# Kernel tuning notes

Hardware: AMD Instinct MI355X
Metric: run time of the kernel (lower is better)

The kernel has to match this reference:

```python
import jax, jax.numpy as jnp
import numpy as np
import math

FACTOR = 5


def setup_inputs() -> dict:
    key = jax.random.key(0)
    k1, k2, k3, k4 = jax.random.split(key, 4)
    B, L, H, D = 8, 1024, 8, 64
    S = FACTOR * math.ceil(math.log(L))  # U_part = 35
    return {
        "queries": jax.random.normal(k1, (B, L, H, D), jnp.float32),
        "keys": jax.random.normal(k2, (B, L, H, D), jnp.float32),
        "values": jax.random.normal(k3, (B, L, H, D), jnp.float32),
        "sample_idx": jax.random.randint(k4, (L, S), 0, L, dtype=jnp.int32),
        "attn_mask": 0,  # unused by the original forward
    }


def reference(queries, keys, values, sample_idx, attn_mask):
    B, L_Q, H, D = queries.shape
    L_K = keys.shape[1]
    # [B, L, H, D] -> [B, H, L, D]
    Q = jnp.transpose(queries, (0, 2, 1, 3))
    K = jnp.transpose(keys, (0, 2, 1, 3))
    V = jnpp_transpose(values) if False else jnp.transpose(values, (0, 2, 1, 3))

    u = min(FACTOR * math.ceil(math.log(L_Q)), L_Q)  # n_top

    # --- _prob_QK: sampled scores, sparsity measure, top-u query selection ---
    K_sample = K[:, :, sample_idx, :]  # [B, H, L_Q, S, D]
    QK_sample = jnp.einsum('bhqd,bhqsd->bhqs', Q, K_sample)  # [B, H, L_Q, S]
    M = QK_sample.max(axis=-1) - QK_sample.sum(axis=-1) / L_K  # [B, H, L_Q]
    _, M_top = jax.lax.top_k(M, u)  # [B, H, u]

    Q_reduce = jnp.take_along_axis(Q, M_top[..., None], axis=2)  # [B, H, u, D]
    scale = 1.0 / math.sqrt(D)
    scores_top = jnp.einsum('bhud,bhkd->bhuk', Q_reduce, K) * scale  # [B, H, u, L_K]

    # --- initial context (mask_flag=True): running causal mean of V ---
    denom = jnp.arange(1, L_K + 1, dtype=V.dtype)[:, None]  # [L_K, 1]
    context = jnp.cumsum(V, axis=2) / denom  # [B, H, L_K, D]

    # --- softmax over keys, sparse update of selected query rows ---
    attn = jax.nn.softmax(scores_top, axis=-1)  # [B, H, u, L_K]
    update = jnp.einsum('bhuk,bhkd->bhud', attn, V)  # [B, H, u, D]

    b_idx = jnp.arange(B)[:, None, None]
    h_idx = jnp.arange(H)[None, :, None]
    context = context.at[b_idx, h_idx, M_top].set(update)

    return jnp.transpose(context, (0, 2, 1, 3))  # [B, L_Q, H, D]
```

## Files before the change

### kernel.cpp

```cpp
#include <hip/hip_runtime.h>
#include <math.h>

#define BB 8
#define LL 1024
#define HH 8
#define DD 64
#define SS 35
#define UU 35
#define BH (BB*HH)
#define CH 32
#define CROWS (LL/CH)
#define NCHK 4
#define CHK 256
#define RPAD 48

#define MBLOCKS (BB*LL)
#define C1BLOCKS (BH*CH)

typedef __attribute__((ext_vector_type(8))) short short8;
typedef __attribute__((ext_vector_type(4))) float f32x4;

__device__ __forceinline__ size_t qkv_off(int b, int l, int h, int d) {
    return (((size_t)b*LL + l)*HH + h)*DD + d;
}

__device__ __forceinline__ unsigned short f2bf(float x) {
    unsigned int u = __float_as_uint(x);
    u = (u + 0x7fffu + ((u >> 16) & 1u)) >> 16;
    return (unsigned short)u;
}

__device__ __forceinline__ short8 ld_bf8_g(const float* __restrict__ p) {
    float4 x = *reinterpret_cast<const float4*>(p);
    float4 y = *reinterpret_cast<const float4*>(p + 4);
    short8 r;
    r[0] = (short)f2bf(x.x); r[1] = (short)f2bf(x.y);
    r[2] = (short)f2bf(x.z); r[3] = (short)f2bf(x.w);
    r[4] = (short)f2bf(y.x); r[5] = (short)f2bf(y.y);
    r[6] = (short)f2bf(y.z); r[7] = (short)f2bf(y.w);
    return r;
}

__device__ __forceinline__ float red8_shr(float p) {
    int t;
    t = __builtin_amdgcn_update_dpp(0, __float_as_int(p), 0x111, 0xF, 0xF, true);
    p += __int_as_float(t);
    t = __builtin_amdgcn_update_dpp(0, __float_as_int(p), 0x112, 0xF, 0xF, true);
    p += __int_as_float(t);
    t = __builtin_amdgcn_update_dpp(0, __float_as_int(p), 0x114, 0xF, 0xF, true);
    p += __int_as_float(t);
    return p;
}

__global__ __launch_bounds__(512, 2) void kernel_M_csum1(const float* __restrict__ Q,
                                                         const float* __restrict__ K,
                                                         const float* __restrict__ V,
                                                         const int*   __restrict__ sidx,
                                                         float* __restrict__ M,
                                                         float* __restrict__ csum) {
    int blk = blockIdx.x;
    if (blk < MBLOCKS) {
        __shared__ float s_mx[8][8];
        __shared__ float s_sm[8][8];
        int b = blk & 7;
        int q = blk >> 3;
        int tid = threadIdx.x;
        int w = tid >> 6, lane = tid & 63;
        int h = lane >> 3, j = lane & 7, dsub = j * 4;

        const float* qb = Q + ((size_t)(b * LL + q) * HH + h) * DD + dsub;
        f32x4 q0 = *reinterpret_cast<const f32x4*>(qb);
        f32x4 q1 = *reinterpret_cast<const f32x4*>(qb + 32);

        const int* sq = sidx + q * SS;
        int sl[5];
#pragma unroll
        for (int i = 0; i < 5; i++) {
            int s = w + 8 * i;
            sl[i] = sq[s < SS ? s : 0];
        }

        const float* kbase = K + (size_t)b * (LL * HH * DD) + h * DD + dsub;
        f32x4 ka[5], kc[5];
#pragma unroll
        for (int i = 0; i < 5; i++) {
            const float* kp = kbase + (size_t)sl[i] * (HH * DD);
            ka[i] = *reinterpret_cast<const f32x4*>(kp);
            kc[i] = *reinterpret_cast<const f32x4*>(kp + 32);
        }

        float mx = -INFINITY, sm = 0.f;
#pragma unroll
        for (int i = 0; i < 5; i++) {
            float d = q0.x * ka[i].x + q0.y * ka[i].y + q0.z * ka[i].z + q0.w * ka[i].w
                    + q1.x * kc[i].x + q1.y * kc[i].y + q1.z * kc[i].z + q1.w * kc[i].w;
            d = red8_shr(d);
            bool valid = (i < 4) || (w < 3);
            if (valid) { mx = fmaxf(mx, d); sm += d; }
        }
        if (j == 7) { s_mx[w][h] = mx; s_sm[w][h] = sm; }
        __syncthreads();
        if (tid < 8) {
            float m2 = -INFINITY, s2 = 0.f;
#pragma unroll
            for (int ww = 0; ww < 8; ww++) {
                m2 = fmaxf(m2, s_mx[ww][tid]);
                s2 += s_sm[ww][tid];
            }
            M[(b * HH + tid) * LL + q] = m2 - s2 * (1.0f / LL);
        }
    } else {
        int blk2 = blk - MBLOCKS;
        int bh = blk2 >> 5, c = blk2 & (CH - 1);
        int b = bh >> 3, h = bh & 7;
        int d = threadIdx.x & 63, seg = threadIdx.x >> 6;
        int l0 = c * CROWS + seg * 4;
        const float* vp = V + qkv_off(b, l0, h, d);
        float vr[4];
#pragma unroll
        for (int i = 0; i < 4; i++) vr[i] = vp[(size_t)i * (HH * DD)];
        float s = (vr[0] + vr[1]) + (vr[2] + vr[3]);
        __shared__ float red[8][64];
        red[seg][d] = s;
        __syncthreads();
        if (seg == 0) {
            float t = 0.f;
#pragma unroll
            for (int k = 0; k < 8; k++) t += red[k][d];
            csum[(size_t)blk2 * 64 + d] = t;
        }
    }
}

__global__ __launch_bounds__(64, 4) void kernel_topk_csum2(const float* __restrict__ M,
                                                           int* __restrict__ top,
                                                           const float* __restrict__ V,
                                                           const float* __restrict__ csum,
                                                           float* __restrict__ out) {
    if (blockIdx.x < BH) {
        int bh = blockIdx.x, lane = threadIdx.x;
        float v[16];
#pragma unroll
        for (int i = 0; i < 16; i++) v[i] = M[bh * LL + i * 64 + lane];

        for (int k = 0; k < UU; k++) {
            float bv = -INFINITY; int bi = 0x7fffffff;
#pragma unroll
            for (int i = 0; i < 16; i++) {
                if (v[i] > bv) { bv = v[i]; bi = i * 64 + lane; }
            }
#pragma unroll
            for (int w = 1; w < 64; w <<= 1) {
                float ov = __shfl_xor(bv, w);
                int   oi = __shfl_xor(bi, w);
                if (ov > bv || (ov == bv && oi < bi)) { bv = ov; bi = oi; }
            }
            if (lane == 0) top[bh * UU + k] = bi;
            if ((bi & 63) == lane) {
                int slot = bi >> 6;
#pragma unroll
                for (int i = 0; i < 16; i++) if (i == slot) v[i] = -INFINITY;
            }
        }
    } else {
        int blk = blockIdx.x - BH;
        int bh = blk >> 5, c = blk & (CH - 1);
        int b = bh >> 3, h = bh & 7;
        int d = threadIdx.x;
        int l0 = c * CROWS;
        const float* vp = V + qkv_off(b, l0, h, d);

        float vr[CROWS];
#pragma unroll
        for (int i = 0; i < CROWS; i++) vr[i] = vp[(size_t)i * (HH * DD)];

        float prefix = 0.f;
#pragma unroll
        for (int cc = 0; cc < CH; cc++) {
            float vv = csum[(size_t)(bh * CH + cc) * 64 + d];
            prefix += (cc < c) ? vv : 0.f;
        }
        float* op = out + qkv_off(b, l0, h, d);
        float run = prefix;
#pragma unroll
        for (int i = 0; i < CROWS; i++) {
            run += vr[i];
            op[(size_t)i * (HH * DD)] = run / (float)(l0 + i + 1);
        }
    }
}

__global__ __launch_bounds__(256) void kernel_attn_part(const float* __restrict__ Q,
                                                        const float* __restrict__ K,
                                                        const float* __restrict__ V,
                                                        const int*   __restrict__ top,
                                                        float* __restrict__ m_ws,
                                                        float* __restrict__ se_ws,
                                                        float* __restrict__ pv_ws) {
    __shared__ unsigned short vt[64 * CHK];
    __shared__ unsigned short p_lds[RPAD * CHK];
    __shared__ float red_m[4][RPAD];
    __shared__ float red_se[4][RPAD];
    __shared__ int   qpos_s[RPAD];

    const int blk = blockIdx.x;
    const int bh  = blk >> 2;
    const int ch  = blk & 3;
    const int b   = bh >> 3, h = bh & 7;
    const int l0  = ch * CHK;
    const int tid = threadIdx.x;
    const int w    = tid >> 6;
    const int lane = tid & 63;
    const int c    = lane & 15;
    const int g    = lane >> 4;
    const float scale = 0.125f;

    if (tid < RPAD) qpos_s[tid] = top[bh * UU + (tid < UU ? tid : UU - 1)];

#pragma unroll
    for (int i = 0; i < 8; i++) {
        int task = i * 256 + tid;
        int d   = task & 63;
        int lq8 = task >> 6;
        float vv[8];
#pragma unroll
        for (int j = 0; j < 8; j++)
            vv[j] = V[qkv_off(b, l0 + lq8 * 8 + j, h, d)];
        short8 pk;
#pragma unroll
        for (int j = 0; j < 8; j++) pk[j] = (short)f2bf(vv[j]);
        *reinterpret_cast<short8*>(vt + d * CHK + (((lq8 ^ (d & 31)) << 3))) = pk;
    }
    __syncthreads();

    f32x4 acc[3][4];
#pragma unroll
    for (int mt = 0; mt < 3; mt++)
#pragma unroll
        for (int nt = 0; nt < 4; nt++) acc[mt][nt] = (f32x4){0.f, 0.f, 0.f, 0.f};

#pragma unroll
    for (int ks = 0; ks < 2; ks++) {
        int k0 = ks * 32 + g * 8;
        short8 af[3];
#pragma unroll
        for (int mt = 0; mt < 3; mt++) {
            int row = mt * 16 + c;
            af[mt] = ld_bf8_g(Q + qkv_off(b, qpos_s[row], h, k0));
        }
#pragma unroll
        for (int nt = 0; nt < 4; nt++) {
            int kl = l0 + w * 64 + nt * 16 + c;
            short8 bf = ld_bf8_g(K + qkv_off(b, kl, h, k0));
#pragma unroll
            for (int mt = 0; mt < 3; mt++)
                acc[mt][nt] = __builtin_amdgcn_mfma_f32_16x16x32_bf16(af[mt], bf, acc[mt][nt], 0, 0, 0);
        }
    }

    float tmax[3][4];
#pragma unroll
    for (int mt = 0; mt < 3; mt++)
#pragma unroll
        for (int r = 0; r < 4; r++) {
            float m = fmaxf(fmaxf(acc[mt][0][r], acc[mt][1][r]),
                            fmaxf(acc[mt][2][r], acc[mt][3][r]));
            m = fmaxf(m, __shfl_xor(m, 1));
            m = fmaxf(m, __shfl_xor(m, 2));
            m = fmaxf(m, __shfl_xor(m, 4));
            m = fmaxf(m, __shfl_xor(m, 8));
            tmax[mt][r] = m;
        }
    if (c == 0) {
#pragma unroll
        for (int mt = 0; mt < 3; mt++)
#pragma unroll
            for (int r = 0; r < 4; r++)
                red_m[w][mt * 16 + g * 4 + r] = tmax[mt][r];
    }
    __syncthreads();

    float tse[3][4];
#pragma unroll
    for (int mt = 0; mt < 3; mt++)
#pragma unroll
        for (int r = 0; r < 4; r++) {
            int row = mt * 16 + g * 4 + r;
            float m = fmaxf(fmaxf(red_m[0][row], red_m[1][row]),
                            fmaxf(red_m[2][row], red_m[3][row]));
            float s = 0.f;
#pragma unroll
            for (int nt = 0; nt < 4; nt++) {
                float p = __expf(scale * (acc[mt][nt][r] - m));
                acc[mt][nt][r] = p;
                s += p;
                p_lds[row * CHK + w * 64 + nt * 16 + c] = f2bf(p);
            }
            s += __shfl_xor(s, 1);
            s += __shfl_xor(s, 2);
            s += __shfl_xor(s, 4);
            s += __shfl_xor(s, 8);
            tse[mt][r] = s;
        }
    if (c == 0) {
#pragma unroll
        for (int mt = 0; mt < 3; mt++)
#pragma unroll
            for (int r = 0; r < 4; r++)
                red_se[w][mt * 16 + g * 4 + r] = tse[mt][r];
    }
    __syncthreads();

    if (tid < RPAD) {
        float mm = fmaxf(fmaxf(red_m[0][tid], red_m[1][tid]),
                         fmaxf(red_m[2][tid], red_m[3][tid]));
        float ss = red_se[0][tid] + red_se[1][tid] + red_se[2][tid] + red_se[3][tid];
        m_ws[blk * RPAD + tid]  = mm;
        se_ws[blk * RPAD + tid] = ss;
    }

    f32x4 acc2[3];
#pragma unroll
    for (int mt = 0; mt < 3; mt++) acc2[mt] = (f32x4){0.f, 0.f, 0.f, 0.f};

#pragma unroll
    for (int ks = 0; ks < 8; ks++) {
        int slot = ks * 4 + g;
        int d    = w * 16 + c;
        short8 bf = *reinterpret_cast<const short8*>(
            vt + d * CHK + ((slot ^ (d & 31)) << 3));
#pragma unroll
        for (int mt = 0; mt < 3; mt++) {
            short8 af = *reinterpret_cast<const short8*>(
                p_lds + (mt * 16 + c) * CHK + ks * 32 + g * 8);
            acc2[mt] = __builtin_amdgcn_mfma_f32_16x16x32_bf16(af, bf, acc2[mt], 0, 0, 0);
        }
    }

#pragma unroll
    for (int mt = 0; mt < 3; mt++)
#pragma unroll
        for (int r = 0; r < 4; r++) {
            int row = mt * 16 + g * 4 + r;
            pv_ws[((size_t)blk * RPAD + row) * 64 + w * 16 + c] = acc2[mt][r];
        }
}

__global__ __launch_bounds__(256) void kernel_attn_comb(const int* __restrict__ top,
                                                        const float* __restrict__ m_ws,
                                                        const float* __restrict__ se_ws,
                                                        const float* __restrict__ pv_ws,
                                                        float* __restrict__ out) {
    int bh = blockIdx.x;
    int b = bh >> 3, h = bh & 7;
    const float scale = 0.125f;
    for (int idx = threadIdx.x; idx < UU * 64; idx += 256) {
        int r = idx >> 6, d = idx & 63;
        float mc[NCHK];
        float mm = -INFINITY;
#pragma unroll
        for (int ch = 0; ch < NCHK; ch++) {
            mc[ch] = m_ws[(bh * NCHK + ch) * RPAD + r];
            mm = fmaxf(mm, mc[ch]);
        }
        float num = 0.f, den = 0.f;
#pragma unroll
        for (int ch = 0; ch < NCHK; ch++) {
            float f = __expf(scale * (mc[ch] - mm));
            num += f * pv_ws[((size_t)(bh * NCHK + ch) * RPAD + r) * 64 + d];
            den += f * se_ws[(bh * NCHK + ch) * RPAD + r];
        }
        out[qkv_off(b, top[bh * UU + r], h, d)] = num / den;
    }
}

extern "C" void kernel_launch(void* const* d_in, const int* in_sizes, int n_in,
                              void* d_out, int out_size, void* d_ws, size_t ws_size,
                              hipStream_t stream) {
    const float* Q    = (const float*)d_in[0];
    const float* K    = (const float*)d_in[1];
    const float* V    = (const float*)d_in[2];
    const int*   sidx = (const int*)d_in[3];
    float* out = (float*)d_out;

    char* ws = (char*)d_ws;
    float* M     = (float*)(ws);
    int*   top   = (int*)  (ws + 262144);
    float* csum  = (float*)(ws + 271360);
    float* m_ws  = (float*)(ws + 795648);
    float* se_ws = (float*)(ws + 844800);
    float* pv_ws = (float*)(ws + 893952);

    kernel_M_csum1   <<<MBLOCKS + C1BLOCKS, 512, 0, stream>>>(Q, K, V, sidx, M, csum);
    kernel_topk_csum2<<<BH + C1BLOCKS, 64, 0, stream>>>(M, top, V, csum, out);
    kernel_attn_part <<<BH * NCHK, 256, 0, stream>>>(Q, K, V, top, m_ws, se_ws, pv_ws);
    kernel_attn_comb <<<BH, 256, 0, stream>>>(top, m_ws, se_ws, pv_ws, out);
}
```

Before: 80.89 us.

## Fuse top-k, split-K attention and combine into one online-softmax kernel; single-block cumsum

Cuts the launch chain from four kernels to two. The causal-mean cumsum now runs as 64 blocks that each scan a whole (b,h) column in 8 segments of 128 rows, and these blocks are co-scheduled with the M computation. The top-k selection is folded into the attention kernel, which runs one block per (b,h) and loops over the four key chunks with an online softmax, removing the partial-result workspace and the combine kernel. This saves launch gaps and workspace traffic. In exchange, attention parallelism drops from 256 blocks to 64, and the serial 35-step top-k plus per-chunk syncs sit on the critical path.

New measurement: 109.9 us. 35.9% more time.

```diff
diff --git a/kernel.cpp b/kernel.cpp
--- a/kernel.cpp
+++ b/kernel.cpp
@@ -8,14 +8,12 @@
 #define SS 35
 #define UU 35
 #define BH (BB*HH)
-#define CH 32
-#define CROWS (LL/CH)
 #define NCHK 4
 #define CHK 256
 #define RPAD 48
 
+#define CSBLOCKS BH
 #define MBLOCKS (BB*LL)
-#define C1BLOCKS (BH*CH)
 
 typedef __attribute__((ext_vector_type(8))) short short8;
 typedef __attribute__((ext_vector_type(4))) float f32x4;
@@ -52,18 +50,44 @@
     return p;
 }
 
-__global__ __launch_bounds__(512, 2) void kernel_M_csum1(const float* __restrict__ Q,
-                                                         const float* __restrict__ K,
-                                                         const float* __restrict__ V,
-                                                         const int*   __restrict__ sidx,
-                                                         float* __restrict__ M,
-                                                         float* __restrict__ csum) {
+__global__ __launch_bounds__(512, 2) void kernel_M_cumsum(const float* __restrict__ Q,
+                                                          const float* __restrict__ K,
+                                                          const float* __restrict__ V,
+                                                          const int*   __restrict__ sidx,
+                                                          float* __restrict__ M,
+                                                          float* __restrict__ out) {
     int blk = blockIdx.x;
-    if (blk < MBLOCKS) {
+    if (blk < CSBLOCKS) {
+        __shared__ float partial[8][64];
+        int bh = blk;
+        int b = bh >> 3, h = bh & 7;
+        int d = threadIdx.x & 63, seg = threadIdx.x >> 6;
+        int l0 = seg * 128;
+        const float* vp = V + qkv_off(b, l0, h, d);
+
+        float s = 0.f;
+#pragma unroll 8
+        for (int i = 0; i < 128; i++) s += vp[(size_t)i * (HH * DD)];
+        partial[seg][d] = s;
+        __syncthreads();
+        float run = 0.f;
+#pragma unroll
+        for (int ss = 0; ss < 7; ss++) {
+            float v = partial[ss][d];
+            run += (ss < seg) ? v : 0.f;
+        }
+        float* op = out + qkv_off(b, l0, h, d);
+#pragma unroll 8
+        for (int i = 0; i < 128; i++) {
+            run += vp[(size_t)i * (HH * DD)];
+            op[(size_t)i * (HH * DD)] = run / (float)(l0 + i + 1);
+        }
+    } else {
         __shared__ float s_mx[8][8];
         __shared__ float s_sm[8][8];
-        int b = blk & 7;
-        int q = blk >> 3;
+        int mblk = blk - CSBLOCKS;
+        int b = mblk & 7;
+        int q = mblk >> 3;
         int tid = threadIdx.x;
         int w = tid >> 6, lane = tid & 63;
         int h = lane >> 3, j = lane & 7, dsub = j * 4;
@@ -109,105 +133,23 @@
             }
             M[(b * HH + tid) * LL + q] = m2 - s2 * (1.0f / LL);
         }
-    } else {
-        int blk2 = blk - MBLOCKS;
-        int bh = blk2 >> 5, c = blk2 & (CH - 1);
-        int b = bh >> 3, h = bh & 7;
-        int d = threadIdx.x & 63, seg = threadIdx.x >> 6;
-        int l0 = c * CROWS + seg * 4;
-        const float* vp = V + qkv_off(b, l0, h, d);
-        float vr[4];
-#pragma unroll
-        for (int i = 0; i < 4; i++) vr[i] = vp[(size_t)i * (HH * DD)];
-        float s = (vr[0] + vr[1]) + (vr[2] + vr[3]);
-        __shared__ float red[8][64];
-        red[seg][d] = s;
-        __syncthreads();
-        if (seg == 0) {
-            float t = 0.f;
-#pragma unroll
-            for (int k = 0; k < 8; k++) t += red[k][d];
-            csum[(size_t)blk2 * 64 + d] = t;
-        }
     }
 }
 
-__global__ __launch_bounds__(64, 4) void kernel_topk_csum2(const float* __restrict__ M,
-                                                           int* __restrict__ top,
-                                                           const float* __restrict__ V,
-                                                           const float* __restrict__ csum,
-                                                           float* __restrict__ out) {
-    if (blockIdx.x < BH) {
-        int bh = blockIdx.x, lane = threadIdx.x;
-        float v[16];
-#pragma unroll
-        for (int i = 0; i < 16; i++) v[i] = M[bh * LL + i * 64 + lane];
-
-        for (int k = 0; k < UU; k++) {
-            float bv = -INFINITY; int bi = 0x7fffffff;
-#pragma unroll
-            for (int i = 0; i < 16; i++) {
-                if (v[i] > bv) { bv = v[i]; bi = i * 64 + lane; }
-            }
-#pragma unroll
-            for (int w = 1; w < 64; w <<= 1) {
-                float ov = __shfl_xor(bv, w);
-                int   oi = __shfl_xor(bi, w);
-                if (ov > bv || (ov == bv && oi < bi)) { bv = ov; bi = oi; }
-            }
-            if (lane == 0) top[bh * UU + k] = bi;
-            if ((bi & 63) == lane) {
-                int slot = bi >> 6;
-#pragma unroll
-                for (int i = 0; i < 16; i++) if (i == slot) v[i] = -INFINITY;
-            }
-        }
-    } else {
-        int blk = blockIdx.x - BH;
-        int bh = blk >> 5, c = blk & (CH - 1);
-        int b = bh >> 3, h = bh & 7;
-        int d = threadIdx.x;
-        int l0 = c * CROWS;
-        const float* vp = V + qkv_off(b, l0, h, d);
-
-        float vr[CROWS];
-#pragma unroll
-        for (int i = 0; i < CROWS; i++) vr[i] = vp[(size_t)i * (HH * DD)];
-
-        float prefix = 0.f;
-#pragma unroll
-        for (int cc = 0; cc < CH; cc++) {
-            float vv = csum[(size_t)(bh * CH + cc) * 64 + d];
-            prefix += (cc < c) ? vv : 0.f;
-        }
-        float* op = out + qkv_off(b, l0, h, d);
-        float run = prefix;
-#pragma unroll
-        for (int i = 0; i < CROWS; i++) {
-            run += vr[i];
-            op[(size_t)i * (HH * DD)] = run / (float)(l0 + i + 1);
-        }
-    }
-}
-
-__global__ __launch_bounds__(256) void kernel_attn_part(const float* __restrict__ Q,
-                                                        const float* __restrict__ K,
-                                                        const float* __restrict__ V,
-                                                        const int*   __restrict__ top,
-                                                        float* __restrict__ m_ws,
-                                                        float* __restrict__ se_ws,
-                                                        float* __restrict__ pv_ws) {
+__global__ __launch_bounds__(256) void kernel_attn(const float* __restrict__ Q,
+                                                   const float* __restrict__ K,
+                                                   const float* __restrict__ V,
+                                                   const float* __restrict__ M,
+                                                   float* __restrict__ out) {
     __shared__ unsigned short vt[64 * CHK];
     __shared__ unsigned short p_lds[RPAD * CHK];
     __shared__ float red_m[4][RPAD];
     __shared__ float red_se[4][RPAD];
+    __shared__ float m_run[RPAD], se_run[RPAD], f_s[RPAD];
     __shared__ int   qpos_s[RPAD];
 
-    const int blk = blockIdx.x;
-    const int bh  = blk >> 2;
-    const int ch  = blk & 3;
+    const int bh  = blockIdx.x;
     const int b   = bh >> 3, h = bh & 7;
-    const int l0  = ch * CHK;
     const int tid = threadIdx.x;
     const int w    = tid >> 6;
     const int lane = tid & 63;
@@ -215,163 +157,166 @@
     const int g    = lane >> 4;
     const float scale = 0.125f;
 
-    if (tid < RPAD) qpos_s[tid] = top[bh * UU + (tid < UU ? tid : UU - 1)];
-
-#pragma unroll
-    for (int i = 0; i < 8; i++) {
-        int task = i * 256 + tid;
-        int d   = task & 63;
-        int lq8 = task >> 6;
-        float vv[8];
-#pragma unroll
-        for (int j = 0; j < 8; j++)
-            vv[j] = V[qkv_off(b, l0 + lq8 * 8 + j, h, d)];
-        short8 pk;
-#pragma unroll
-        for (int j = 0; j < 8; j++) pk[j] = (short)f2bf(vv[j]);
-        *reinterpret_cast<short8*>(vt + d * CHK + (((lq8 ^ (d & 31)) << 3))) = pk;
+    if (w == 0) {
+        float v[16];
+#pragma unroll
+        for (int i = 0; i < 16; i++) v[i] = M[bh * LL + i * 64 + lane];
+        int last = 0;
+        for (int k = 0; k < UU; k++) {
+            float bv = -INFINITY; int bi = 0x7fffffff;
+#pragma unroll
+            for (int i = 0; i < 16; i++) {
+                if (v[i] > bv) { bv = v[i]; bi = i * 64 + lane; }
+            }
+#pragma unroll
+            for (int x = 1; x < 64; x <<= 1) {
+                float ov = __shfl_xor(bv, x);
+                int   oi = __shfl_xor(bi, x);
+                if (ov > bv || (ov == bv && oi < bi)) { bv = ov; bi = oi; }
+            }
+            if (lane == 0) qpos_s[k] = bi;
+            if (k == UU - 1) last = bi;
+            if ((bi & 63) == lane) {
+                int slot = bi >> 6;
+#pragma unroll
+                for (int i = 0; i < 16; i++) if (i == slot) v[i] = -INFINITY;
+            }
+        }
+        if (lane >= UU && lane < RPAD) qpos_s[lane] = last;
+    } else if (w == 1 && lane < RPAD) {
+        m_run[lane] = -INFINITY;
+        se_run[lane] = 0.f;
     }
     __syncthreads();
 
-    f32x4 acc[3][4];
-#pragma unroll
-    for (int mt = 0; mt < 3; mt++)
-#pragma unroll
-        for (int nt = 0; nt < 4; nt++) acc[mt][nt] = (f32x4){0.f, 0.f, 0.f, 0.f};
-
-#pragma unroll
-    for (int ks = 0; ks < 2; ks++) {
-        int k0 = ks * 32 + g * 8;
-        short8 af[3];
-#pragma unroll
-        for (int mt = 0; mt < 3; mt++) {
-            int row = mt * 16 + c;
-            af[mt] = ld_bf8_g(Q + qkv_off(b, qpos_s[row], h, k0));
-        }
-#pragma unroll
-        for (int nt = 0; nt < 4; nt++) {
-            int kl = l0 + w * 64 + nt * 16 + c;
-            short8 bf = ld_bf8_g(K + qkv_off(b, kl, h, k0));
-#pragma unroll
-            for (int mt = 0; mt < 3; mt++)
-                acc[mt][nt] = __builtin_amdgcn_mfma_f32_16x16x32_bf16(af[mt], bf, acc[mt][nt], 0, 0, 0);
-        }
+    f32x4 acc2[3];
+#pragma unroll
+    for (int mt = 0; mt < 3; mt++) acc2[mt] = (f32x4){0.f, 0.f, 0.f, 0.f};
+
+    for (int ch = 0; ch < NCHK; ch++) {
+        const int l0 = ch * CHK;
+
+#pragma unroll
+        for (int i = 0; i < 8; i++) {
+            int task = i * 256 + tid;
+            int d   = task & 63;
+            int lq8 = task >> 6;
+            float vv[8];
+#pragma unroll
+            for (int jj = 0; jj < 8; jj++)
+                vv[jj] = V[qkv_off(b, l0 + lq8 * 8 + jj, h, d)];
+            short8 pk;
+#pragma unroll
+            for (int jj = 0; jj < 8; jj++) pk[jj] = (short)f2bf(vv[jj]);
+            *reinterpret_cast<short8*>(vt + d * CHK + (((lq8 ^ (d & 31)) << 3))) = pk;
+        }
+        __syncthreads();
+
+        f32x4 acc[3][4];
+#pragma unroll
+        for (int mt = 0; mt < 3; mt++)
+#pragma unroll
+            for (int nt = 0; nt < 4; nt++) acc[mt][nt] = (f32x4){0.f, 0.f, 0.f, 0.f};
+
+#pragma unroll
+        for (int ks = 0; ks < 2; ks++) {
+            int k0 = ks * 32 + g * 8;
+            short8 af[3];
+#pragma unroll
+            for (int mt = 0; mt < 3; mt++) {
+                int row = mt * 16 + c;
+                af[mt] = ld_bf8_g(Q + qkv_off(b, qpos_s[row], h, k0));
+            }
+#pragma unroll
+            for (int nt = 0; nt < 4; nt++) {
+                int kl = l0 + w * 64 + nt * 16 + c;
+                short8 bf = ld_bf8_g(K + qkv_off(b, kl, h, k0));
+#pragma unroll
+                for (int mt = 0; mt < 3; mt++)
+                    acc[mt][nt] = __builtin_amdgcn_mfma_f32_16x16x32_bf16(af[mt], bf, acc[mt][nt], 0, 0, 0);
+            }
+        }
+
+#pragma unroll
+        for (int mt = 0; mt < 3; mt++)
+#pragma unroll
+            for (int r = 0; r < 4; r++) {
+                float m = fmaxf(fmaxf(acc[mt][0][r], acc[mt][1][r]),
+                                fmaxf(acc[mt][2][r], acc[mt][3][r]));
+                m = fmaxf(m, __shfl_xor(m, 1));
+                m = fmaxf(m, __shfl_xor(m, 2));
+                m = fmaxf(m, __shfl_xor(m, 4));
+                m = fmaxf(m, __shfl_xor(m, 8));
+                if (c == 0) red_m[w][mt * 16 + g * 4 + r] = m;
+            }
+        __syncthreads();
+
+#pragma unroll
+        for (int mt = 0; mt < 3; mt++)
+#pragma unroll
+            for (int r = 0; r < 4; r++) {
+                int row = mt * 16 + g * 4 + r;
+                float mc = fmaxf(fmaxf(red_m[0][row], red_m[1][row]),
+                                 fmaxf(red_m[2][row], red_m[3][row]));
+                float mnew = fmaxf(m_run[row], mc);
+                float s = 0.f;
+#pragma unroll
+                for (int nt = 0; nt < 4; nt++) {
+                    float p = __expf(scale * (acc[mt][nt][r] - mnew));
+                    s += p;
+                    p_lds[row * CHK + w * 64 + nt * 16 + c] = f2bf(p);
+                }
+                s += __shfl_xor(s, 1);
+                s += __shfl_xor(s, 2);
+                s += __shfl_xor(s, 4);
+                s += __shfl_xor(s, 8);
+                if (c == 0) red_se[w][row] = s;
+            }
+        __syncthreads();
+
+        if (tid < RPAD) {
+            float mold = m_run[tid];
+            float mc = fmaxf(fmaxf(red_m[0][tid], red_m[1][tid]),
+                             fmaxf(red_m[2][tid], red_m[3][tid]));
+            float mnew = fmaxf(mold, mc);
+            float f = __expf(scale * (mold - mnew));
+            se_run[tid] = se_run[tid] * f +
+                          (red_se[0][tid] + red_se[1][tid] + red_se[2][tid] + red_se[3][tid]);
+            m_run[tid] = mnew;
+            f_s[tid] = f;
+        }
+        __syncthreads();
+
+#pragma unroll
+        for (int mt = 0; mt < 3; mt++)
+#pragma unroll
+            for (int r = 0; r < 4; r++)
+                acc2[mt][r] *= f_s[mt * 16 + g * 4 + r];
+
+#pragma unroll
+        for (int ks = 0; ks < 8; ks++) {
+            int slot = ks * 4 + g;
+            int d    = w * 16 + c;
+            short8 bf = *reinterpret_cast<const short8*>(
+                vt + d * CHK + ((slot ^ (d & 31)) << 3));
+#pragma unroll
+            for (int mt = 0; mt < 3; mt++) {
+                short8 af = *reinterpret_cast<const short8*>(
+                    p_lds + (mt * 16 + c) * CHK + ks * 32 + g * 8);
+                acc2[mt] = __builtin_amdgcn_mfma_f32_16x16x32_bf16(af, bf, acc2[mt], 0, 0, 0);
+            }
+        }
+        __syncthreads();
     }
 
-    float tmax[3][4];
-#pragma unroll
-    for (int mt = 0; mt < 3; mt++)
-#pragma unroll
-        for (int r = 0; r < 4; r++) {
-            float m = fmaxf(fmaxf(acc[mt][0][r], acc[mt][1][r]),
-                            fmaxf(acc[mt][2][r], acc[mt][3][r]));
-            m = fmaxf(m, __shfl_xor(m, 1));
-            m = fmaxf(m, __shfl_xor(m, 2));
-            m = fmaxf(m, __shfl_xor(m, 4));
-            m = fmaxf(m, __shfl_xor(m, 8));
-            tmax[mt][r] = m;
-        }
-    if (c == 0) {
-#pragma unroll
-        for (int mt = 0; mt < 3; mt++)
-#pragma unroll
-            for (int r = 0; r < 4; r++)
-                red_m[w][mt * 16 + g * 4 + r] = tmax[mt][r];
-    }
-    __syncthreads();
-
-    float tse[3][4];
 #pragma unroll
     for (int mt = 0; mt < 3; mt++)
 #pragma unroll
         for (int r = 0; r < 4; r++) {
             int row = mt * 16 + g * 4 + r;
-            float m = fmaxf(fmaxf(red_m[0][row], red_m[1][row]),
-                            fmaxf(red_m[2][row], red_m[3][row]));
-            float s = 0.f;
-#pragma unroll
-            for (int nt = 0; nt < 4; nt++) {
-                float p = __expf(scale * (acc[mt][nt][r] - m));
-                acc[mt][nt][r] = p;
-                s += p;
-                p_lds[row * CHK + w * 64 + nt * 16 + c] = f2bf(p);
-            }
-            s += __shfl_xor(s, 1);
-            s += __shfl_xor(s, 2);
-            s += __shfl_xor(s, 4);
-            s += __shfl_xor(s, 8);
-            tse[mt][r] = s;
-        }
-    if (c == 0) {
-#pragma unroll
-        for (int mt = 0; mt < 3; mt++)
-#pragma unroll
-            for (int r = 0; r < 4; r++)
-                red_se[w][mt * 16 + g * 4 + r] = tse[mt][r];
-    }
-    __syncthreads();
-
-    if (tid < RPAD) {
-        float mm = fmaxf(fmaxf(red_m[0][tid], red_m[1][tid]),
-                         fmaxf(red_m[2][tid], red_m[3][tid]));
-        float ss = red_se[0][tid] + red_se[1][tid] + red_se[2][tid] + red_se[3][tid];
-        m_ws[blk * RPAD + tid]  = mm;
-        se_ws[blk * RPAD + tid] = ss;
-    }
-
-    f32x4 acc2[3];
-#pragma unroll
-    for (int mt = 0; mt < 3; mt++) acc2[mt] = (f32x4){0.f, 0.f, 0.f, 0.f};
-
-#pragma unroll
-    for (int ks = 0; ks < 8; ks++) {
-        int slot = ks * 4 + g;
-        int d    = w * 16 + c;
-        short8 bf = *reinterpret_cast<const short8*>(
-            vt + d * CHK + ((slot ^ (d & 31)) << 3));
-#pragma unroll
-        for (int mt = 0; mt < 3; mt++) {
-            short8 af = *reinterpret_cast<const short8*>(
-                p_lds + (mt * 16 + c) * CHK + ks * 32 + g * 8);
-            acc2[mt] = __builtin_amdgcn_mfma_f32_16x16x32_bf16(af, bf, acc2[mt], 0, 0, 0);
-        }
-    }
-
-#pragma unroll
-    for (int mt = 0; mt < 3; mt++)
-#pragma unroll
-        for (int r = 0; r < 4; r++) {
-            int row = mt * 16 + g * 4 + r;
-            pv_ws[((size_t)blk * RPAD + row) * 64 + w * 16 + c] = acc2[mt][r];
-        }
-}
-
-__global__ __launch_bounds__(256) void kernel_attn_comb(const int* __restrict__ top,
-                                                        const float* __restrict__ m_ws,
-                                                        const float* __restrict__ se_ws,
-                                                        const float* __restrict__ pv_ws,
-                                                        float* __restrict__ out) {
-    int bh = blockIdx.x;
-    int b = bh >> 3, h = bh & 7;
-    const float scale = 0.125f;
-    for (int idx = threadIdx.x; idx < UU * 64; idx += 256) {
-        int r = idx >> 6, d = idx & 63;
-        float mc[NCHK];
-        float mm = -INFINITY;
-#pragma unroll
-        for (int ch = 0; ch < NCHK; ch++) {
-            mc[ch] = m_ws[(bh * NCHK + ch) * RPAD + r];
-            mm = fmaxf(mm, mc[ch]);
-        }
-        float num = 0.f, den = 0.f;
-#pragma unroll
-        for (int ch = 0; ch < NCHK; ch++) {
-            float f = __expf(scale * (mc[ch] - mm));
-            num += f * pv_ws[((size_t)(bh * NCHK + ch) * RPAD + r) * 64 + d];
-            den += f * se_ws[(bh * NCHK + ch) * RPAD + r];
-        }
-        out[qkv_off(b, top[bh * UU + r], h, d)] = num / den;
-    }
+            if (row < UU)
+                out[qkv_off(b, qpos_s[row], h, w * 16 + c)] = acc2[mt][r] / se_run[row];
+        }
 }
 
 extern "C" void kernel_launch(void* const* d_in, const int* in_sizes, int n_in,
@@ -383,16 +328,8 @@
     const int*   sidx = (const int*)d_in[3];
     float* out = (float*)d_out;
 
-    char* ws = (char*)d_ws;
-    float* M     = (float*)(ws);
-    int*   top   = (int*)  (ws + 262144);
-    float* csum  = (float*)(ws + 271360);
-    float* m_ws  = (float*)(ws + 795648);
-    float* se_ws = (float*)(ws + 844800);
-    float* pv_ws = (float*)(ws + 893952);
-
-    kernel_M_csum1   <<<MBLOCKS + C1BLOCKS, 512, 0, stream>>>(Q, K, V, sidx, M, csum);
-    kernel_topk_csum2<<<BH + C1BLOCKS, 64, 0, stream>>>(M, top, V, csum, out);
-    kernel_attn_part <<<BH * NCHK, 256, 0, stream>>>(Q, K, V, top, m_ws, se_ws, pv_ws);
-    kernel_attn_comb <<<BH, 256, 0, stream>>>(top, m_ws, se_ws, pv_ws, out);
-}
+    float* M = (float*)d_ws;
+
+    kernel_M_cumsum<<<CSBLOCKS + MBLOCKS, 512, 0, stream>>>(Q, K, V, sidx, M, out);
+    kernel_attn    <<<BH, 256, 0, stream>>>(Q, K, V, M, out);
+}
```
